# Performance work log

Hardware: AMD Instinct MI355X
Metric: run time of the kernel (lower is better)

The kernel has to match this reference:

```python
import jax, jax.numpy as jnp
import numpy as np

IN_DIM, DIM, HEADS = 128, 32, 4
L, B = 256, 1


def setup_inputs() -> dict:
    key = jax.random.key(0)
    ks = jax.random.split(key, 10)
    z = jax.random.normal(ks[0], (B, L, L, IN_DIM), dtype=jnp.float32)
    src_mask = jax.random.randint(ks[1], (B, L), 0, 2, dtype=jnp.int32)
    s = 1.0 / np.sqrt(IN_DIM)
    return {
        "z": z,
        "ln_gamma": jnp.ones((IN_DIM,), jnp.float32),
        "ln_beta": jnp.zeros((IN_DIM,), jnp.float32),
        "w_qkv": jax.random.normal(ks[2], (IN_DIM, 3 * HEADS * DIM), jnp.float32) * s,
        "w_pair": jax.random.normal(ks[3], (IN_DIM, HEADS), jnp.float32) * s,
        "w_gate": jax.random.normal(ks[4], (IN_DIM, IN_DIM), jnp.float32) * s,
        "b_gate": jax.random.normal(ks[5], (IN_DIM,), jnp.float32) * 0.02,
        "w_out": jax.random.normal(ks[6], (HEADS * DIM, IN_DIM), jnp.float32) * s,
        "b_out": jax.random.normal(ks[7], (IN_DIM,), jnp.float32) * 0.02,
        "src_mask": src_mask,
    }


def reference(z, ln_gamma, ln_beta, w_qkv, w_pair, w_gate, b_gate, w_out, b_out, src_mask):
    b, i, j, c = z.shape
    h, d = HEADS, DIM
    # mask: zeros -> -1, then outer product -> [b, L, L]
    m = jnp.where(src_mask == 0, -1, src_mask).astype(z.dtype)
    attn_mask = m[:, :, None] * m[:, None, :]
    # LayerNorm over channel dim (eps=1e-5, as nn.LayerNorm default)
    mu = jnp.mean(z, axis=-1, keepdims=True)
    var = jnp.mean((z - mu) ** 2, axis=-1, keepdims=True)
    zn = (z - mu) * jax.lax.rsqrt(var + 1e-5) * ln_gamma + ln_beta
    # qkv projection (no bias), split into heads
    qkv = zn @ w_qkv  # [b,i,j,3*h*d]
    q, k, v = jnp.split(qkv, 3, axis=-1)
    q = q.reshape(b, i, j, h, d)
    k = k.reshape(b, i, j, h, d)
    v = v.reshape(b, i, j, h, d)
    bias = zn @ w_pair  # [b,i,j,h]
    gate = jax.nn.sigmoid(zn @ w_gate + b_gate)  # [b,i,j,c]
    scale = jnp.asarray(d, z.dtype) ** 0.5
    # row-wise attention: attend along j within each row r=i
    logits = jnp.einsum('brihd,brjhd->brijh', q, k) / scale + bias[:, None]
    logits = jnp.where(attn_mask[:, None, :, :, None] == -1, jnp.asarray(-1e-9, z.dtype), logits)
    attn = jax.nn.softmax(logits, axis=3)
    out = jnp.einsum('brijh,brjhd->brihd', attn, v).reshape(b, i, j, h * d)
    out = gate * out
    return out @ w_out + b_out
```

## Files before the change

kernel.cpp:

```cpp
#include <hip/hip_runtime.h>
#include <hip/hip_bf16.h>
#include <math.h>

typedef __attribute__((ext_vector_type(4))) short short4v;
typedef __attribute__((ext_vector_type(8))) short short8v;
typedef __attribute__((ext_vector_type(4))) float f32x4;

#define QB_OFF    0
#define KB_OFF    16777216
#define VB_OFF    33554432
#define BIAS_OFF  50331648
#define GATEB_OFF 51380224
#define ATTB_OFF  68157440
#define WT_OFF    84934656
#define WOT_OFF   85065728

static __device__ __forceinline__ short f2bf(float x) {
    __hip_bfloat16 h = __float2bfloat16(x);
    return *reinterpret_cast<short*>(&h);
}
static __device__ __forceinline__ float bf2f(short x) {
    __hip_bfloat16 h = *reinterpret_cast<__hip_bfloat16*>(&x);
    return __bfloat162float(h);
}
static __device__ __forceinline__ unsigned int pk2(float a, float b) {
    return (unsigned int)(unsigned short)f2bf(a)
         | ((unsigned int)(unsigned short)f2bf(b) << 16);
}

__global__ __launch_bounds__(128) void k_prep_w(
    const float* __restrict__ w_qkv, const float* __restrict__ w_gate,
    const float* __restrict__ w_out, __hip_bfloat16* __restrict__ wT,
    __hip_bfloat16* __restrict__ woT)
{
    const int n = blockIdx.x, k = threadIdx.x;
    if (n < 384)      wT[n*128 + k]        = __float2bfloat16(w_qkv[k*384 + n]);
    else if (n < 512) wT[n*128 + k]        = __float2bfloat16(w_gate[k*128 + (n-384)]);
    else              woT[(n-512)*128 + k] = __float2bfloat16(w_out[k*128 + (n-512)]);
}

__global__ __launch_bounds__(256) void k1_ln_proj(
    const float* __restrict__ z, const float* __restrict__ gamma,
    const float* __restrict__ beta, const float* __restrict__ w_pair,
    const float* __restrict__ b_gate, const int* __restrict__ src_mask,
    const __hip_bfloat16* __restrict__ wT,
    __hip_bfloat16* __restrict__ qb, __hip_bfloat16* __restrict__ kb,
    __hip_bfloat16* __restrict__ vb, float* __restrict__ biasf,
    __hip_bfloat16* __restrict__ gateb)
{
    const int tid = threadIdx.x;
    const int lane = tid & 63, wv = tid >> 6;
    const int l15 = lane & 15, lg4 = lane >> 4;
    const int tokbase = blockIdx.x * 128 + wv * 32;

    float zn[2][32];
    float s[2] = {0.f, 0.f}, s2[2] = {0.f, 0.f};
    #pragma unroll
    for (int mt = 0; mt < 2; ++mt) {
        const float* zp = z + (size_t)(tokbase + mt*16 + l15) * 128 + lg4*8;
        #pragma unroll
        for (int ks = 0; ks < 4; ++ks) {
            float4 a = *(const float4*)(zp + ks*32);
            float4 b = *(const float4*)(zp + ks*32 + 4);
            zn[mt][ks*8+0] = a.x; zn[mt][ks*8+1] = a.y;
            zn[mt][ks*8+2] = a.z; zn[mt][ks*8+3] = a.w;
            zn[mt][ks*8+4] = b.x; zn[mt][ks*8+5] = b.y;
            zn[mt][ks*8+6] = b.z; zn[mt][ks*8+7] = b.w;
            s[mt]  += a.x + a.y + a.z + a.w + b.x + b.y + b.z + b.w;
            s2[mt] += a.x*a.x + a.y*a.y + a.z*a.z + a.w*a.w
                    + b.x*b.x + b.y*b.y + b.z*b.z + b.w*b.w;
        }
    }
    #pragma unroll
    for (int mt = 0; mt < 2; ++mt) {
        s[mt]  += __shfl_xor(s[mt], 16);  s[mt]  += __shfl_xor(s[mt], 32);
        s2[mt] += __shfl_xor(s2[mt], 16); s2[mt] += __shfl_xor(s2[mt], 32);
    }

    #pragma unroll
    for (int ks = 0; ks < 4; ++ks) {
        float4 g0 = *(const float4*)(gamma + ks*32 + lg4*8);
        float4 g1 = *(const float4*)(gamma + ks*32 + lg4*8 + 4);
        float4 b0 = *(const float4*)(beta  + ks*32 + lg4*8);
        float4 b1 = *(const float4*)(beta  + ks*32 + lg4*8 + 4);
        float gg[8] = {g0.x,g0.y,g0.z,g0.w,g1.x,g1.y,g1.z,g1.w};
        float bb[8] = {b0.x,b0.y,b0.z,b0.w,b1.x,b1.y,b1.z,b1.w};
        #pragma unroll
        for (int mt = 0; mt < 2; ++mt) {
            const float mu  = s[mt] * (1.f/128.f);
            const float inv = rsqrtf(s2[mt]*(1.f/128.f) - mu*mu + 1e-5f);
            #pragma unroll
            for (int e = 0; e < 8; ++e)
                zn[mt][ks*8+e] = (zn[mt][ks*8+e] - mu) * inv * gg[e] + bb[e];
        }
    }

    {
        float pr[2][4] = {{0,0,0,0},{0,0,0,0}};
        #pragma unroll
        for (int ks = 0; ks < 4; ++ks)
            #pragma unroll
            for (int e = 0; e < 8; ++e) {
                float4 wp = *(const float4*)(w_pair + (ks*32 + lg4*8 + e)*4);
                #pragma unroll
                for (int mt = 0; mt < 2; ++mt) {
                    const float a = zn[mt][ks*8+e];
                    pr[mt][0] = fmaf(a, wp.x, pr[mt][0]);
                    pr[mt][1] = fmaf(a, wp.y, pr[mt][1]);
                    pr[mt][2] = fmaf(a, wp.z, pr[mt][2]);
                    pr[mt][3] = fmaf(a, wp.w, pr[mt][3]);
                }
            }
        #pragma unroll
        for (int mt = 0; mt < 2; ++mt)
            #pragma unroll
            for (int h = 0; h < 4; ++h) {
                pr[mt][h] += __shfl_xor(pr[mt][h], 16);
                pr[mt][h] += __shfl_xor(pr[mt][h], 32);
            }
        if (lg4 == 0) {
            #pragma unroll
            for (int mt = 0; mt < 2; ++mt) {
                const int t = tokbase + mt*16 + l15;
                const int i = t >> 8, j = t & 255;
                const bool masked = (src_mask[i] == 0) != (src_mask[j] == 0);
                #pragma unroll
                for (int h = 0; h < 4; ++h)
                    biasf[(size_t)(h*256 + i)*256 + j] = masked ? 1e30f : pr[mt][h];
            }
        }
    }

    short8v afr[2][4];
    #pragma unroll
    for (int mt = 0; mt < 2; ++mt)
        #pragma unroll
        for (int ks = 0; ks < 4; ++ks) {
            short8v f;
            #pragma unroll
            for (int e = 0; e < 8; ++e) f[e] = f2bf(zn[mt][ks*8+e]);
            afr[mt][ks] = f;
        }

    const ushort* wTu = (const ushort*)wT;
    for (int ch = 0; ch < 8; ++ch) {
        f32x4 acc[2][4];
        #pragma unroll
        for (int mt = 0; mt < 2; ++mt)
            #pragma unroll
            for (int nt = 0; nt < 4; ++nt) acc[mt][nt] = (f32x4){0.f,0.f,0.f,0.f};
        const ushort* Bb = wTu + (size_t)ch * 64 * 128;
        #pragma unroll
        for (int ks = 0; ks < 4; ++ks)
            #pragma unroll
            for (int nt = 0; nt < 4; ++nt) {
                short8v bfr = *(const short8v*)(Bb + (nt*16 + l15)*128 + ks*32 + lg4*8);
                acc[0][nt] = __builtin_amdgcn_mfma_f32_16x16x32_bf16(bfr, afr[0][ks], acc[0][nt], 0,0,0);
                acc[1][nt] = __builtin_amdgcn_mfma_f32_16x16x32_bf16(bfr, afr[1][ks], acc[1][nt], 0,0,0);
            }
        if (ch < 6) {
            __hip_bfloat16* dstb = (ch < 2 ? qb : (ch < 4 ? kb : vb));
            ushort* dst = (ushort*)dstb;
            #pragma unroll
            for (int mt = 0; mt < 2; ++mt) {
                const int t = tokbase + mt*16 + l15;
                const int i = t >> 8, j = t & 255;
                #pragma unroll
                for (int nt = 0; nt < 4; ++nt) {
                    const int h  = (ch & 1)*2 + (nt >> 1);
                    const int d0 = (nt & 1)*16 + lg4*4;
                    uint2 v;
                    v.x = pk2(acc[mt][nt][0], acc[mt][nt][1]);
                    v.y = pk2(acc[mt][nt][2], acc[mt][nt][3]);
                    *(uint2*)(dst + ((size_t)((i*4 + h)*256 + j))*32 + d0) = v;
                }
            }
        } else {
            ushort* gdst = (ushort*)gateb;
            #pragma unroll
            for (int mt = 0; mt < 2; ++mt) {
                const int t = tokbase + mt*16 + l15;
                #pragma unroll
                for (int nt = 0; nt < 4; ++nt) {
                    const int c0 = (ch - 6)*64 + nt*16 + lg4*4;
                    float4 bg = *(const float4*)(b_gate + c0);
                    const float g0 = 1.f / (1.f + __expf(-(acc[mt][nt][0] + bg.x)));
                    const float g1 = 1.f / (1.f + __expf(-(acc[mt][nt][1] + bg.y)));
                    const float g2 = 1.f / (1.f + __expf(-(acc[mt][nt][2] + bg.z)));
                    const float g3 = 1.f / (1.f + __expf(-(acc[mt][nt][3] + bg.w)));
                    uint2 v;
                    v.x = pk2(g0, g1);
                    v.y = pk2(g2, g3);
                    *(uint2*)(gdst + (size_t)t*128 + c0) = v;
                }
            }
        }
    }
}

__global__ __launch_bounds__(128) void k_attn_mfma(
    const __hip_bfloat16* __restrict__ qb_, const __hip_bfloat16* __restrict__ kb_,
    const __hip_bfloat16* __restrict__ vb_, const float* __restrict__ biasf,
    __hip_bfloat16* __restrict__ attb)
{
    __shared__ __align__(16) char klds[256 * 80];
    const int tid  = threadIdx.x;
    const int lane = tid & 63;
    const int wv   = tid >> 6;
    const int h = blockIdx.x >> 8, r = blockIdx.x & 255;
    const int rh = r * 4 + h;
    const int l15 = lane & 15, lg4 = lane >> 4;

    const ushort* qg = (const ushort*)qb_ + (size_t)rh * 8192;
    const ushort* kg = (const ushort*)kb_ + (size_t)rh * 8192;
    const ushort* vg = (const ushort*)vb_ + (size_t)rh * 8192;

    short4v vfrag[16][2];
    #pragma unroll
    for (int jt = 0; jt < 16; ++jt)
        #pragma unroll
        for (int dt = 0; dt < 2; ++dt) {
            short4v f;
            #pragma unroll
            for (int e = 0; e < 4; ++e)
                f[e] = (short)vg[(size_t)(jt*16 + lg4*4 + e)*32 + dt*16 + l15];
            vfrag[jt][dt] = f;
        }

    #pragma unroll
    for (int t = 0; t < 8; ++t) {
        uint4 kv = *(const uint4*)(kg + t*1024 + tid*8);
        *(uint4*)(klds + (t*32 + (tid >> 2))*80 + (tid & 3)*16) = kv;
    }
    __syncthreads();

    const float inv_scale = 0.17677669529663687f;

    for (int ii = 0; ii < 8; ++ii) {
        const int it = wv*8 + ii;
        short8v qf = *(const short8v*)(qg + (it*16 + l15)*32 + lg4*8);

        f32x4 s[16];
        #pragma unroll
        for (int jt = 0; jt < 16; ++jt) {
            short8v kf = *(const short8v*)(klds + (jt*16 + l15)*80 + lg4*16);
            s[jt] = __builtin_amdgcn_mfma_f32_16x16x32_bf16(
                        kf, qf, (f32x4){0.f,0.f,0.f,0.f}, 0, 0, 0);
        }

        const float* bp = biasf + (size_t)(h*256 + it*16 + l15) * 256;
        #pragma unroll
        for (int jt = 0; jt < 16; ++jt) {
            f32x4 bv = *(const f32x4*)(bp + jt*16 + lg4*4);
            #pragma unroll
            for (int e = 0; e < 4; ++e)
                s[jt][e] = (bv[e] > 1e29f) ? -1e-9f : fmaf(s[jt][e], inv_scale, bv[e]);
        }

        float m = -INFINITY;
        #pragma unroll
        for (int jt = 0; jt < 16; ++jt) {
            const float a = fmaxf(fmaxf(s[jt][0], s[jt][1]),
                                  fmaxf(s[jt][2], s[jt][3]));
            m = fmaxf(m, a);
        }
        m = fmaxf(m, __shfl_xor(m, 16));
        m = fmaxf(m, __shfl_xor(m, 32));

        float lsum = 0.f;
        #pragma unroll
        for (int jt = 0; jt < 16; ++jt)
            #pragma unroll
            for (int e = 0; e < 4; ++e) {
                const float p = __expf(s[jt][e] - m);
                s[jt][e] = p;
                lsum += p;
            }
        lsum += __shfl_xor(lsum, 16);
        lsum += __shfl_xor(lsum, 32);
        const float invl = 1.f / lsum;

        short4v pa[16];
        #pragma unroll
        for (int jt = 0; jt < 16; ++jt) {
            short4v t4;
            t4[0] = f2bf(s[jt][0] * invl); t4[1] = f2bf(s[jt][1] * invl);
            t4[2] = f2bf(s[jt][2] * invl); t4[3] = f2bf(s[jt][3] * invl);
            pa[jt] = t4;
        }

        f32x4 o0 = {0.f,0.f,0.f,0.f}, o1 = {0.f,0.f,0.f,0.f};
        #pragma unroll
        for (int jt = 0; jt < 16; ++jt) {
            o0 = __builtin_amdgcn_mfma_f32_16x16x16bf16_1k(vfrag[jt][0], pa[jt], o0, 0, 0, 0);
            o1 = __builtin_amdgcn_mfma_f32_16x16x16bf16_1k(vfrag[jt][1], pa[jt], o1, 0, 0, 0);
        }

        ushort* op = (ushort*)attb + (size_t)(r*256 + it*16 + l15)*128 + h*32 + lg4*4;
        uint2 v0, v1;
        v0.x = pk2(o0[0], o0[1]); v0.y = pk2(o0[2], o0[3]);
        v1.x = pk2(o1[0], o1[1]); v1.y = pk2(o1[2], o1[3]);
        *(uint2*)(op)      = v0;
        *(uint2*)(op + 16) = v1;
    }
}

__global__ __launch_bounds__(256) void k3_out_proj(
    const __hip_bfloat16* __restrict__ gateb, const __hip_bfloat16* __restrict__ attb,
    const __hip_bfloat16* __restrict__ woT, const float* __restrict__ b_out,
    float* __restrict__ out)
{
    const int tid = threadIdx.x;
    const int lane = tid & 63, wv = tid >> 6;
    const int l15 = lane & 15, lg4 = lane >> 4;
    const int tokbase = blockIdx.x * 64 + wv * 16;

    const ushort* gu = (const ushort*)gateb;
    const ushort* au = (const ushort*)attb;

    short8v afr[4];
    #pragma unroll
    for (int ks = 0; ks < 4; ++ks) {
        const size_t base = (size_t)(tokbase + l15)*128 + ks*32 + lg4*8;
        short8v gv = *(const short8v*)(gu + base);
        short8v av = *(const short8v*)(au + base);
        short8v p;
        #pragma unroll
        for (int e = 0; e < 8; ++e) p[e] = f2bf(bf2f(gv[e]) * bf2f(av[e]));
        afr[ks] = p;
    }

    const ushort* wo = (const ushort*)woT;
    const int t = tokbase + l15;
    for (int ch = 0; ch < 2; ++ch) {
        f32x4 acc[4];
        #pragma unroll
        for (int nt = 0; nt < 4; ++nt) acc[nt] = (f32x4){0.f,0.f,0.f,0.f};
        const ushort* Bb = wo + (size_t)ch * 64 * 128;
        #pragma unroll
        for (int ks = 0; ks < 4; ++ks)
            #pragma unroll
            for (int nt = 0; nt < 4; ++nt) {
                short8v bfr = *(const short8v*)(Bb + (nt*16 + l15)*128 + ks*32 + lg4*8);
                acc[nt] = __builtin_amdgcn_mfma_f32_16x16x32_bf16(bfr, afr[ks], acc[nt], 0,0,0);
            }
        #pragma unroll
        for (int nt = 0; nt < 4; ++nt) {
            const int n0 = ch*64 + nt*16 + lg4*4;
            float4 bo = *(const float4*)(b_out + n0);
            float4 v;
            v.x = acc[nt][0] + bo.x;
            v.y = acc[nt][1] + bo.y;
            v.z = acc[nt][2] + bo.z;
            v.w = acc[nt][3] + bo.w;
            *(float4*)(out + (size_t)t*128 + n0) = v;
        }
    }
}

extern "C" void kernel_launch(void* const* d_in, const int* in_sizes, int n_in,
                              void* d_out, int out_size, void* d_ws, size_t ws_size,
                              hipStream_t stream)
{
    const float* z       = (const float*)d_in[0];
    const float* gamma   = (const float*)d_in[1];
    const float* beta    = (const float*)d_in[2];
    const float* w_qkv   = (const float*)d_in[3];
    const float* w_pair  = (const float*)d_in[4];
    const float* w_gate  = (const float*)d_in[5];
    const float* b_gate  = (const float*)d_in[6];
    const float* w_out   = (const float*)d_in[7];
    const float* b_out   = (const float*)d_in[8];
    const int*   src_mask= (const int*)d_in[9];
    float* out = (float*)d_out;
    char*  wsb = (char*)d_ws;

    __hip_bfloat16* qb    = (__hip_bfloat16*)(wsb + QB_OFF);
    __hip_bfloat16* kb    = (__hip_bfloat16*)(wsb + KB_OFF);
    __hip_bfloat16* vb    = (__hip_bfloat16*)(wsb + VB_OFF);
    float*          biasf = (float*)(wsb + BIAS_OFF);
    __hip_bfloat16* gateb = (__hip_bfloat16*)(wsb + GATEB_OFF);
    __hip_bfloat16* attb  = (__hip_bfloat16*)(wsb + ATTB_OFF);
    __hip_bfloat16* wT    = (__hip_bfloat16*)(wsb + WT_OFF);
    __hip_bfloat16* woT   = (__hip_bfloat16*)(wsb + WOT_OFF);

    hipLaunchKernelGGL(k_prep_w, dim3(640), dim3(128), 0, stream,
                       w_qkv, w_gate, w_out, wT, woT);
    hipLaunchKernelGGL(k1_ln_proj, dim3(512), dim3(256), 0, stream,
                       z, gamma, beta, w_pair, b_gate, src_mask, wT,
                       qb, kb, vb, biasf, gateb);
    hipLaunchKernelGGL(k_attn_mfma, dim3(1024), dim3(128), 0, stream,
                       qb, kb, vb, biasf, attb);
    hipLaunchKernelGGL(k3_out_proj, dim3(1024), dim3(256), 0, stream,
                       gateb, attb, woT, b_out, out);
}
```

Before: 128.6 us.

## Halve per-wave work in LN projection and stage V transposed in LDS for attention

The LN/projection kernel now handles one 16-token M tile per wave instead of two, doubles its grid and adds a min-blocks launch bound, which cuts register pressure so more waves can be resident. The attention kernel moves to 256 threads per block with 4 query tiles per wave. V is now written transposed into shared memory once, instead of each wave gathering V fragments from global memory with scalar strided loads into registers. This trades extra LDS traffic and reuse of each weight fragment across fewer tokens for higher occupancy and coalesced V loads.

```diff
diff --git a/kernel.cpp b/kernel.cpp
--- a/kernel.cpp
+++ b/kernel.cpp
@@ -39,7 +39,7 @@
     else              woT[(n-512)*128 + k] = __float2bfloat16(w_out[k*128 + (n-512)]);
 }
 
-__global__ __launch_bounds__(256) void k1_ln_proj(
+__global__ __launch_bounds__(256, 4) void k1_ln_proj(
     const float* __restrict__ z, const float* __restrict__ gamma,
     const float* __restrict__ beta, const float* __restrict__ w_pair,
     const float* __restrict__ b_gate, const int* __restrict__ src_mask,
@@ -51,31 +51,28 @@
     const int tid = threadIdx.x;
     const int lane = tid & 63, wv = tid >> 6;
     const int l15 = lane & 15, lg4 = lane >> 4;
-    const int tokbase = blockIdx.x * 128 + wv * 32;
-
-    float zn[2][32];
-    float s[2] = {0.f, 0.f}, s2[2] = {0.f, 0.f};
-    #pragma unroll
-    for (int mt = 0; mt < 2; ++mt) {
-        const float* zp = z + (size_t)(tokbase + mt*16 + l15) * 128 + lg4*8;
+    const int tokbase = blockIdx.x * 64 + wv * 16;
+    const int tok = tokbase + l15;
+
+    float zn[32];
+    float s = 0.f, s2 = 0.f;
+    {
+        const float* zp = z + (size_t)tok * 128 + lg4*8;
         #pragma unroll
         for (int ks = 0; ks < 4; ++ks) {
             float4 a = *(const float4*)(zp + ks*32);
             float4 b = *(const float4*)(zp + ks*32 + 4);
-            zn[mt][ks*8+0] = a.x; zn[mt][ks*8+1] = a.y;
-            zn[mt][ks*8+2] = a.z; zn[mt][ks*8+3] = a.w;
-            zn[mt][ks*8+4] = b.x; zn[mt][ks*8+5] = b.y;
-            zn[mt][ks*8+6] = b.z; zn[mt][ks*8+7] = b.w;
-            s[mt]  += a.x + a.y + a.z + a.w + b.x + b.y + b.z + b.w;
-            s2[mt] += a.x*a.x + a.y*a.y + a.z*a.z + a.w*a.w
-                    + b.x*b.x + b.y*b.y + b.z*b.z + b.w*b.w;
-        }
-    }
-    #pragma unroll
-    for (int mt = 0; mt < 2; ++mt) {
-        s[mt]  += __shfl_xor(s[mt], 16);  s[mt]  += __shfl_xor(s[mt], 32);
-        s2[mt] += __shfl_xor(s2[mt], 16); s2[mt] += __shfl_xor(s2[mt], 32);
-    }
+            zn[ks*8+0] = a.x; zn[ks*8+1] = a.y; zn[ks*8+2] = a.z; zn[ks*8+3] = a.w;
+            zn[ks*8+4] = b.x; zn[ks*8+5] = b.y; zn[ks*8+6] = b.z; zn[ks*8+7] = b.w;
+            s  += a.x + a.y + a.z + a.w + b.x + b.y + b.z + b.w;
+            s2 += a.x*a.x + a.y*a.y + a.z*a.z + a.w*a.w
+                + b.x*b.x + b.y*b.y + b.z*b.z + b.w*b.w;
+        }
+    }
+    s  += __shfl_xor(s, 16);  s  += __shfl_xor(s, 32);
+    s2 += __shfl_xor(s2, 16); s2 += __shfl_xor(s2, 32);
+    const float mu  = s * (1.f/128.f);
+    const float inv = rsqrtf(s2*(1.f/128.f) - mu*mu + 1e-5f);
 
     #pragma unroll
     for (int ks = 0; ks < 4; ++ks) {
@@ -86,124 +83,98 @@
         float gg[8] = {g0.x,g0.y,g0.z,g0.w,g1.x,g1.y,g1.z,g1.w};
         float bb[8] = {b0.x,b0.y,b0.z,b0.w,b1.x,b1.y,b1.z,b1.w};
         #pragma unroll
-        for (int mt = 0; mt < 2; ++mt) {
-            const float mu  = s[mt] * (1.f/128.f);
-            const float inv = rsqrtf(s2[mt]*(1.f/128.f) - mu*mu + 1e-5f);
-            #pragma unroll
-            for (int e = 0; e < 8; ++e)
-                zn[mt][ks*8+e] = (zn[mt][ks*8+e] - mu) * inv * gg[e] + bb[e];
-        }
+        for (int e = 0; e < 8; ++e)
+            zn[ks*8+e] = (zn[ks*8+e] - mu) * inv * gg[e] + bb[e];
     }
 
     {
-        float pr[2][4] = {{0,0,0,0},{0,0,0,0}};
+        float pr[4] = {0,0,0,0};
         #pragma unroll
         for (int ks = 0; ks < 4; ++ks)
             #pragma unroll
             for (int e = 0; e < 8; ++e) {
                 float4 wp = *(const float4*)(w_pair + (ks*32 + lg4*8 + e)*4);
-                #pragma unroll
-                for (int mt = 0; mt < 2; ++mt) {
-                    const float a = zn[mt][ks*8+e];
-                    pr[mt][0] = fmaf(a, wp.x, pr[mt][0]);
-                    pr[mt][1] = fmaf(a, wp.y, pr[mt][1]);
-                    pr[mt][2] = fmaf(a, wp.z, pr[mt][2]);
-                    pr[mt][3] = fmaf(a, wp.w, pr[mt][3]);
-                }
-            }
-        #pragma unroll
-        for (int mt = 0; mt < 2; ++mt)
-            #pragma unroll
-            for (int h = 0; h < 4; ++h) {
-                pr[mt][h] += __shfl_xor(pr[mt][h], 16);
-                pr[mt][h] += __shfl_xor(pr[mt][h], 32);
-            }
+                const float a = zn[ks*8+e];
+                pr[0] = fmaf(a, wp.x, pr[0]);
+                pr[1] = fmaf(a, wp.y, pr[1]);
+                pr[2] = fmaf(a, wp.z, pr[2]);
+                pr[3] = fmaf(a, wp.w, pr[3]);
+            }
+        #pragma unroll
+        for (int h = 0; h < 4; ++h) {
+            pr[h] += __shfl_xor(pr[h], 16);
+            pr[h] += __shfl_xor(pr[h], 32);
+        }
         if (lg4 == 0) {
-            #pragma unroll
-            for (int mt = 0; mt < 2; ++mt) {
-                const int t = tokbase + mt*16 + l15;
-                const int i = t >> 8, j = t & 255;
-                const bool masked = (src_mask[i] == 0) != (src_mask[j] == 0);
-                #pragma unroll
-                for (int h = 0; h < 4; ++h)
-                    biasf[(size_t)(h*256 + i)*256 + j] = masked ? 1e30f : pr[mt][h];
-            }
-        }
-    }
-
-    short8v afr[2][4];
+            const int i = tok >> 8, j = tok & 255;
+            const bool masked = (src_mask[i] == 0) != (src_mask[j] == 0);
+            #pragma unroll
+            for (int h = 0; h < 4; ++h)
+                biasf[(size_t)(h*256 + i)*256 + j] = masked ? 1e30f : pr[h];
+        }
+    }
+
+    short8v afr[4];
     #pragma unroll
-    for (int mt = 0; mt < 2; ++mt)
-        #pragma unroll
-        for (int ks = 0; ks < 4; ++ks) {
-            short8v f;
-            #pragma unroll
-            for (int e = 0; e < 8; ++e) f[e] = f2bf(zn[mt][ks*8+e]);
-            afr[mt][ks] = f;
-        }
+    for (int ks = 0; ks < 4; ++ks) {
+        short8v f;
+        #pragma unroll
+        for (int e = 0; e < 8; ++e) f[e] = f2bf(zn[ks*8+e]);
+        afr[ks] = f;
+    }
 
     const ushort* wTu = (const ushort*)wT;
+    const int ti = tok >> 8, tj = tok & 255;
     for (int ch = 0; ch < 8; ++ch) {
-        f32x4 acc[2][4];
-        #pragma unroll
-        for (int mt = 0; mt < 2; ++mt)
-            #pragma unroll
-            for (int nt = 0; nt < 4; ++nt) acc[mt][nt] = (f32x4){0.f,0.f,0.f,0.f};
+        f32x4 acc[4];
+        #pragma unroll
+        for (int nt = 0; nt < 4; ++nt) acc[nt] = (f32x4){0.f,0.f,0.f,0.f};
         const ushort* Bb = wTu + (size_t)ch * 64 * 128;
         #pragma unroll
         for (int ks = 0; ks < 4; ++ks)
             #pragma unroll
             for (int nt = 0; nt < 4; ++nt) {
                 short8v bfr = *(const short8v*)(Bb + (nt*16 + l15)*128 + ks*32 + lg4*8);
-                acc[0][nt] = __builtin_amdgcn_mfma_f32_16x16x32_bf16(bfr, afr[0][ks], acc[0][nt], 0,0,0);
-                acc[1][nt] = __builtin_amdgcn_mfma_f32_16x16x32_bf16(bfr, afr[1][ks], acc[1][nt], 0,0,0);
+                acc[nt] = __builtin_amdgcn_mfma_f32_16x16x32_bf16(bfr, afr[ks], acc[nt], 0,0,0);
             }
         if (ch < 6) {
             __hip_bfloat16* dstb = (ch < 2 ? qb : (ch < 4 ? kb : vb));
             ushort* dst = (ushort*)dstb;
             #pragma unroll
-            for (int mt = 0; mt < 2; ++mt) {
-                const int t = tokbase + mt*16 + l15;
-                const int i = t >> 8, j = t & 255;
-                #pragma unroll
-                for (int nt = 0; nt < 4; ++nt) {
-                    const int h  = (ch & 1)*2 + (nt >> 1);
-                    const int d0 = (nt & 1)*16 + lg4*4;
-                    uint2 v;
-                    v.x = pk2(acc[mt][nt][0], acc[mt][nt][1]);
-                    v.y = pk2(acc[mt][nt][2], acc[mt][nt][3]);
-                    *(uint2*)(dst + ((size_t)((i*4 + h)*256 + j))*32 + d0) = v;
-                }
+            for (int nt = 0; nt < 4; ++nt) {
+                const int h  = (ch & 1)*2 + (nt >> 1);
+                const int d0 = (nt & 1)*16 + lg4*4;
+                uint2 v;
+                v.x = pk2(acc[nt][0], acc[nt][1]);
+                v.y = pk2(acc[nt][2], acc[nt][3]);
+                *(uint2*)(dst + ((size_t)((ti*4 + h)*256 + tj))*32 + d0) = v;
             }
         } else {
             ushort* gdst = (ushort*)gateb;
             #pragma unroll
-            for (int mt = 0; mt < 2; ++mt) {
-                const int t = tokbase + mt*16 + l15;
-                #pragma unroll
-                for (int nt = 0; nt < 4; ++nt) {
-                    const int c0 = (ch - 6)*64 + nt*16 + lg4*4;
-                    float4 bg = *(const float4*)(b_gate + c0);
-                    const float g0 = 1.f / (1.f + __expf(-(acc[mt][nt][0] + bg.x)));
-                    const float g1 = 1.f / (1.f + __expf(-(acc[mt][nt][1] + bg.y)));
-                    const float g2 = 1.f / (1.f + __expf(-(acc[mt][nt][2] + bg.z)));
-                    const float g3 = 1.f / (1.f + __expf(-(acc[mt][nt][3] + bg.w)));
-                    uint2 v;
-                    v.x = pk2(g0, g1);
-                    v.y = pk2(g2, g3);
-                    *(uint2*)(gdst + (size_t)t*128 + c0) = v;
-                }
-            }
-        }
-    }
-}
-
-__global__ __launch_bounds__(128) void k_attn_mfma(
+            for (int nt = 0; nt < 4; ++nt) {
+                const int c0 = (ch - 6)*64 + nt*16 + lg4*4;
+                float4 bg = *(const float4*)(b_gate + c0);
+                const float g0 = 1.f / (1.f + __expf(-(acc[nt][0] + bg.x)));
+                const float g1 = 1.f / (1.f + __expf(-(acc[nt][1] + bg.y)));
+                const float g2 = 1.f / (1.f + __expf(-(acc[nt][2] + bg.z)));
+                const float g3 = 1.f / (1.f + __expf(-(acc[nt][3] + bg.w)));
+                uint2 v;
+                v.x = pk2(g0, g1);
+                v.y = pk2(g2, g3);
+                *(uint2*)(gdst + (size_t)tok*128 + c0) = v;
+            }
+        }
+    }
+}
+
+__global__ __launch_bounds__(256, 4) void k_attn_mfma(
     const __hip_bfloat16* __restrict__ qb_, const __hip_bfloat16* __restrict__ kb_,
     const __hip_bfloat16* __restrict__ vb_, const float* __restrict__ biasf,
     __hip_bfloat16* __restrict__ attb)
 {
     __shared__ __align__(16) char klds[256 * 80];
+    __shared__ __align__(16) char vlds[32 * 520];
     const int tid  = threadIdx.x;
     const int lane = tid & 63;
     const int wv   = tid >> 6;
@@ -215,29 +186,28 @@
     const ushort* kg = (const ushort*)kb_ + (size_t)rh * 8192;
     const ushort* vg = (const ushort*)vb_ + (size_t)rh * 8192;
 
-    short4v vfrag[16][2];
     #pragma unroll
-    for (int jt = 0; jt < 16; ++jt)
-        #pragma unroll
-        for (int dt = 0; dt < 2; ++dt) {
-            short4v f;
-            #pragma unroll
-            for (int e = 0; e < 4; ++e)
-                f[e] = (short)vg[(size_t)(jt*16 + lg4*4 + e)*32 + dt*16 + l15];
-            vfrag[jt][dt] = f;
-        }
-
-    #pragma unroll
-    for (int t = 0; t < 8; ++t) {
-        uint4 kv = *(const uint4*)(kg + t*1024 + tid*8);
-        *(uint4*)(klds + (t*32 + (tid >> 2))*80 + (tid & 3)*16) = kv;
+    for (int t = 0; t < 4; ++t) {
+        uint4 kv = *(const uint4*)(kg + (size_t)(t*64 + (tid >> 2))*32 + (tid & 3)*8);
+        *(uint4*)(klds + (t*64 + (tid >> 2))*80 + (tid & 3)*16) = kv;
+    }
+    {
+        const int j = tid;
+        uint4 tmp[4];
+        #pragma unroll
+        for (int c = 0; c < 4; ++c)
+            tmp[c] = *(const uint4*)(vg + (size_t)j*32 + c*8);
+        const ushort* vals = (const ushort*)tmp;
+        #pragma unroll
+        for (int d = 0; d < 32; ++d)
+            *(ushort*)(vlds + d*520 + j*2) = vals[d];
     }
     __syncthreads();
 
     const float inv_scale = 0.17677669529663687f;
 
-    for (int ii = 0; ii < 8; ++ii) {
-        const int it = wv*8 + ii;
+    for (int ii = 0; ii < 4; ++ii) {
+        const int it = wv*4 + ii;
         short8v qf = *(const short8v*)(qg + (it*16 + l15)*32 + lg4*8);
 
         f32x4 s[16];
@@ -280,20 +250,16 @@
         lsum += __shfl_xor(lsum, 32);
         const float invl = 1.f / lsum;
 
-        short4v pa[16];
+        f32x4 o0 = {0.f,0.f,0.f,0.f}, o1 = {0.f,0.f,0.f,0.f};
         #pragma unroll
         for (int jt = 0; jt < 16; ++jt) {
-            short4v t4;
-            t4[0] = f2bf(s[jt][0] * invl); t4[1] = f2bf(s[jt][1] * invl);
-            t4[2] = f2bf(s[jt][2] * invl); t4[3] = f2bf(s[jt][3] * invl);
-            pa[jt] = t4;
-        }
-
-        f32x4 o0 = {0.f,0.f,0.f,0.f}, o1 = {0.f,0.f,0.f,0.f};
-        #pragma unroll
-        for (int jt = 0; jt < 16; ++jt) {
-            o0 = __builtin_amdgcn_mfma_f32_16x16x16bf16_1k(vfrag[jt][0], pa[jt], o0, 0, 0, 0);
-            o1 = __builtin_amdgcn_mfma_f32_16x16x16bf16_1k(vfrag[jt][1], pa[jt], o1, 0, 0, 0);
+            short4v pa;
+            pa[0] = f2bf(s[jt][0] * invl); pa[1] = f2bf(s[jt][1] * invl);
+            pa[2] = f2bf(s[jt][2] * invl); pa[3] = f2bf(s[jt][3] * invl);
+            short4v vf0 = *(const short4v*)(vlds + (     l15)*520 + (jt*16 + lg4*4)*2);
+            short4v vf1 = *(const short4v*)(vlds + (16 + l15)*520 + (jt*16 + lg4*4)*2);
+            o0 = __builtin_amdgcn_mfma_f32_16x16x16bf16_1k(vf0, pa, o0, 0, 0, 0);
+            o1 = __builtin_amdgcn_mfma_f32_16x16x16bf16_1k(vf1, pa, o1, 0, 0, 0);
         }
 
         ushort* op = (ushort*)attb + (size_t)(r*256 + it*16 + l15)*128 + h*32 + lg4*4;
@@ -386,10 +352,10 @@
 
     hipLaunchKernelGGL(k_prep_w, dim3(640), dim3(128), 0, stream,
                        w_qkv, w_gate, w_out, wT, woT);
-    hipLaunchKernelGGL(k1_ln_proj, dim3(512), dim3(256), 0, stream,
+    hipLaunchKernelGGL(k1_ln_proj, dim3(1024), dim3(256), 0, stream,
                        z, gamma, beta, w_pair, b_gate, src_mask, wT,
                        qb, kb, vb, biasf, gateb);
-    hipLaunchKernelGGL(k_attn_mfma, dim3(1024), dim3(128), 0, stream,
+    hipLaunchKernelGGL(k_attn_mfma, dim3(1024), dim3(256), 0, stream,
                        qb, kb, vb, biasf, attb);
     hipLaunchKernelGGL(k3_out_proj, dim3(1024), dim3(256), 0, stream,
                        gateb, attb, woT, b_out, out);
```

Result: slower. 218.0 us (+69.5%).

## Store V transposed for vector fragment loads and use exp2 softmax

Applied to the files above, without the earlier changes.

The projection kernel now computes the V chunks with swapped MFMA operands and writes V transposed per row/head as [d][j], so the attention kernel can load V fragments as single 8-byte vector loads instead of four scalar strided gathers. The pair bias and logit scale are pre-multiplied by log2(e) so the softmax can use the hardware exp2 instruction directly. This trades a strided store pattern in the projection kernel for contiguous loads in attention.

```diff
diff --git a/kernel.cpp b/kernel.cpp
--- a/kernel.cpp
+++ b/kernel.cpp
@@ -14,6 +14,8 @@
 #define ATTB_OFF  68157440
 #define WT_OFF    84934656
 #define WOT_OFF   85065728
+
+#define LOG2E 1.4426950408889634f
 
 static __device__ __forceinline__ short f2bf(float x) {
     __hip_bfloat16 h = __float2bfloat16(x);
@@ -45,7 +47,7 @@
     const float* __restrict__ b_gate, const int* __restrict__ src_mask,
     const __hip_bfloat16* __restrict__ wT,
     __hip_bfloat16* __restrict__ qb, __hip_bfloat16* __restrict__ kb,
-    __hip_bfloat16* __restrict__ vb, float* __restrict__ biasf,
+    __hip_bfloat16* __restrict__ vbT, float* __restrict__ biasf,
     __hip_bfloat16* __restrict__ gateb)
 {
     const int tid = threadIdx.x;
@@ -126,7 +128,8 @@
                 const bool masked = (src_mask[i] == 0) != (src_mask[j] == 0);
                 #pragma unroll
                 for (int h = 0; h < 4; ++h)
-                    biasf[(size_t)(h*256 + i)*256 + j] = masked ? 1e30f : pr[mt][h];
+                    biasf[(size_t)(h*256 + i)*256 + j] =
+                        masked ? 1e30f : pr[mt][h] * LOG2E;
             }
         }
     }
@@ -143,55 +146,81 @@
         }
 
     const ushort* wTu = (const ushort*)wT;
+    ushort* vdst = (ushort*)vbT;
     for (int ch = 0; ch < 8; ++ch) {
+        const bool vchunk = (ch == 4) || (ch == 5);
         f32x4 acc[2][4];
         #pragma unroll
         for (int mt = 0; mt < 2; ++mt)
             #pragma unroll
             for (int nt = 0; nt < 4; ++nt) acc[mt][nt] = (f32x4){0.f,0.f,0.f,0.f};
         const ushort* Bb = wTu + (size_t)ch * 64 * 128;
-        #pragma unroll
-        for (int ks = 0; ks < 4; ++ks)
-            #pragma unroll
-            for (int nt = 0; nt < 4; ++nt) {
-                short8v bfr = *(const short8v*)(Bb + (nt*16 + l15)*128 + ks*32 + lg4*8);
-                acc[0][nt] = __builtin_amdgcn_mfma_f32_16x16x32_bf16(bfr, afr[0][ks], acc[0][nt], 0,0,0);
-                acc[1][nt] = __builtin_amdgcn_mfma_f32_16x16x32_bf16(bfr, afr[1][ks], acc[1][nt], 0,0,0);
-            }
-        if (ch < 6) {
-            __hip_bfloat16* dstb = (ch < 2 ? qb : (ch < 4 ? kb : vb));
-            ushort* dst = (ushort*)dstb;
+        if (vchunk) {
+            #pragma unroll
+            for (int ks = 0; ks < 4; ++ks)
+                #pragma unroll
+                for (int nt = 0; nt < 4; ++nt) {
+                    short8v bfr = *(const short8v*)(Bb + (nt*16 + l15)*128 + ks*32 + lg4*8);
+                    acc[0][nt] = __builtin_amdgcn_mfma_f32_16x16x32_bf16(afr[0][ks], bfr, acc[0][nt], 0,0,0);
+                    acc[1][nt] = __builtin_amdgcn_mfma_f32_16x16x32_bf16(afr[1][ks], bfr, acc[1][nt], 0,0,0);
+                }
             #pragma unroll
             for (int mt = 0; mt < 2; ++mt) {
-                const int t = tokbase + mt*16 + l15;
-                const int i = t >> 8, j = t & 255;
+                const int j0 = tokbase + mt*16 + lg4*4;
+                const int i  = j0 >> 8, j = j0 & 255;
                 #pragma unroll
                 for (int nt = 0; nt < 4; ++nt) {
-                    const int h  = (ch & 1)*2 + (nt >> 1);
-                    const int d0 = (nt & 1)*16 + lg4*4;
+                    const int nv = (ch - 4)*64 + nt*16 + l15;
+                    const int h = nv >> 5, d = nv & 31;
                     uint2 v;
                     v.x = pk2(acc[mt][nt][0], acc[mt][nt][1]);
                     v.y = pk2(acc[mt][nt][2], acc[mt][nt][3]);
-                    *(uint2*)(dst + ((size_t)((i*4 + h)*256 + j))*32 + d0) = v;
+                    *(uint2*)(vdst + ((size_t)((i*4 + h)*32 + d))*256 + j) = v;
                 }
             }
         } else {
-            ushort* gdst = (ushort*)gateb;
-            #pragma unroll
-            for (int mt = 0; mt < 2; ++mt) {
-                const int t = tokbase + mt*16 + l15;
+            #pragma unroll
+            for (int ks = 0; ks < 4; ++ks)
                 #pragma unroll
                 for (int nt = 0; nt < 4; ++nt) {
-                    const int c0 = (ch - 6)*64 + nt*16 + lg4*4;
-                    float4 bg = *(const float4*)(b_gate + c0);
-                    const float g0 = 1.f / (1.f + __expf(-(acc[mt][nt][0] + bg.x)));
-                    const float g1 = 1.f / (1.f + __expf(-(acc[mt][nt][1] + bg.y)));
-                    const float g2 = 1.f / (1.f + __expf(-(acc[mt][nt][2] + bg.z)));
-                    const float g3 = 1.f / (1.f + __expf(-(acc[mt][nt][3] + bg.w)));
-                    uint2 v;
-                    v.x = pk2(g0, g1);
-                    v.y = pk2(g2, g3);
-                    *(uint2*)(gdst + (size_t)t*128 + c0) = v;
+                    short8v bfr = *(const short8v*)(Bb + (nt*16 + l15)*128 + ks*32 + lg4*8);
+                    acc[0][nt] = __builtin_amdgcn_mfma_f32_16x16x32_bf16(bfr, afr[0][ks], acc[0][nt], 0,0,0);
+                    acc[1][nt] = __builtin_amdgcn_mfma_f32_16x16x32_bf16(bfr, afr[1][ks], acc[1][nt], 0,0,0);
+                }
+            if (ch < 4) {
+                ushort* dst = (ushort*)(ch < 2 ? qb : kb);
+                #pragma unroll
+                for (int mt = 0; mt < 2; ++mt) {
+                    const int t = tokbase + mt*16 + l15;
+                    const int i = t >> 8, j = t & 255;
+                    #pragma unroll
+                    for (int nt = 0; nt < 4; ++nt) {
+                        const int h  = (ch & 1)*2 + (nt >> 1);
+                        const int d0 = (nt & 1)*16 + lg4*4;
+                        uint2 v;
+                        v.x = pk2(acc[mt][nt][0], acc[mt][nt][1]);
+                        v.y = pk2(acc[mt][nt][2], acc[mt][nt][3]);
+                        *(uint2*)(dst + ((size_t)((i*4 + h)*256 + j))*32 + d0) = v;
+                    }
+                }
+            } else {
+                ushort* gdst = (ushort*)gateb;
+                #pragma unroll
+                for (int mt = 0; mt < 2; ++mt) {
+                    const int t = tokbase + mt*16 + l15;
+                    #pragma unroll
+                    for (int nt = 0; nt < 4; ++nt) {
+                        const int c0 = (ch - 6)*64 + nt*16 + lg4*4;
+                        float4 bg = *(const float4*)(b_gate + c0);
+                        const float g0 = 1.f / (1.f + __expf(-(acc[mt][nt][0] + bg.x)));
+                        const float g1 = 1.f / (1.f + __expf(-(acc[mt][nt][1] + bg.y)));
+                        const float g2 = 1.f / (1.f + __expf(-(acc[mt][nt][2] + bg.z)));
+                        const float g3 = 1.f / (1.f + __expf(-(acc[mt][nt][3] + bg.w)));
+                        uint2 v;
+                        v.x = pk2(g0, g1);
+                        v.y = pk2(g2, g3);
+                        *(uint2*)(gdst + (size_t)t*128 + c0) = v;
+                    }
                 }
             }
         }
@@ -200,7 +229,7 @@
 
 __global__ __launch_bounds__(128) void k_attn_mfma(
     const __hip_bfloat16* __restrict__ qb_, const __hip_bfloat16* __restrict__ kb_,
-    const __hip_bfloat16* __restrict__ vb_, const float* __restrict__ biasf,
+    const __hip_bfloat16* __restrict__ vbT_, const float* __restrict__ biasf,
     __hip_bfloat16* __restrict__ attb)
 {
     __shared__ __align__(16) char klds[256 * 80];
@@ -213,19 +242,14 @@
 
     const ushort* qg = (const ushort*)qb_ + (size_t)rh * 8192;
     const ushort* kg = (const ushort*)kb_ + (size_t)rh * 8192;
-    const ushort* vg = (const ushort*)vb_ + (size_t)rh * 8192;
+    const ushort* vt = (const ushort*)vbT_ + (size_t)rh * 8192;
 
     short4v vfrag[16][2];
     #pragma unroll
     for (int jt = 0; jt < 16; ++jt)
         #pragma unroll
-        for (int dt = 0; dt < 2; ++dt) {
-            short4v f;
-            #pragma unroll
-            for (int e = 0; e < 4; ++e)
-                f[e] = (short)vg[(size_t)(jt*16 + lg4*4 + e)*32 + dt*16 + l15];
-            vfrag[jt][dt] = f;
-        }
+        for (int dt = 0; dt < 2; ++dt)
+            vfrag[jt][dt] = *(const short4v*)(vt + (size_t)(dt*16 + l15)*256 + jt*16 + lg4*4);
 
     #pragma unroll
     for (int t = 0; t < 8; ++t) {
@@ -234,7 +258,7 @@
     }
     __syncthreads();
 
-    const float inv_scale = 0.17677669529663687f;
+    const float scale2 = 0.17677669529663687f * LOG2E;
 
     for (int ii = 0; ii < 8; ++ii) {
         const int it = wv*8 + ii;
@@ -254,7 +278,8 @@
             f32x4 bv = *(const f32x4*)(bp + jt*16 + lg4*4);
             #pragma unroll
             for (int e = 0; e < 4; ++e)
-                s[jt][e] = (bv[e] > 1e29f) ? -1e-9f : fmaf(s[jt][e], inv_scale, bv[e]);
+                s[jt][e] = (bv[e] > 1e29f) ? (-1e-9f * LOG2E)
+                                           : fmaf(s[jt][e], scale2, bv[e]);
         }
 
         float m = -INFINITY;
@@ -272,7 +297,7 @@
         for (int jt = 0; jt < 16; ++jt)
             #pragma unroll
             for (int e = 0; e < 4; ++e) {
-                const float p = __expf(s[jt][e] - m);
+                const float p = __builtin_amdgcn_exp2f(s[jt][e] - m);
                 s[jt][e] = p;
                 lsum += p;
             }
@@ -377,7 +402,7 @@
 
     __hip_bfloat16* qb    = (__hip_bfloat16*)(wsb + QB_OFF);
     __hip_bfloat16* kb    = (__hip_bfloat16*)(wsb + KB_OFF);
-    __hip_bfloat16* vb    = (__hip_bfloat16*)(wsb + VB_OFF);
+    __hip_bfloat16* vbT   = (__hip_bfloat16*)(wsb + VB_OFF);
     float*          biasf = (float*)(wsb + BIAS_OFF);
     __hip_bfloat16* gateb = (__hip_bfloat16*)(wsb + GATEB_OFF);
     __hip_bfloat16* attb  = (__hip_bfloat16*)(wsb + ATTB_OFF);
@@ -388,9 +413,9 @@
                        w_qkv, w_gate, w_out, wT, woT);
     hipLaunchKernelGGL(k1_ln_proj, dim3(512), dim3(256), 0, stream,
                        z, gamma, beta, w_pair, b_gate, src_mask, wT,
-                       qb, kb, vb, biasf, gateb);
+                       qb, kb, vbT, biasf, gateb);
     hipLaunchKernelGGL(k_attn_mfma, dim3(1024), dim3(128), 0, stream,
-                       qb, kb, vb, biasf, attb);
+                       qb, kb, vbT, biasf, attb);
     hipLaunchKernelGGL(k3_out_proj, dim3(1024), dim3(256), 0, stream,
                        gateb, attb, woT, b_out, out);
 }
```

New measurement: 131.6 us. +2.3%, slower.
